# Kernel optimization log

Measured on AMD Instinct MI355X. Metric: run time of the kernel, lower is better.

## Reference

```python
import jax, jax.numpy as jnp
import numpy as np

B, S, D = 4, 4096, 1024

def setup_inputs() -> dict:
    key = jax.random.key(0)
    ks = jax.random.split(key, 11)
    scale = 1.0 / np.sqrt(D)
    def lin(k):
        return jax.random.normal(k, (D, D), dtype=jnp.float32) * scale
    return {
        "x": jax.random.normal(ks[0], (B, S, D), dtype=jnp.float32),
        "Wq": lin(ks[1]), "bq": jax.random.normal(ks[2], (D,), dtype=jnp.float32) * 0.02,
        "Wk": lin(ks[3]), "bk": jax.random.normal(ks[4], (D,), dtype=jnp.float32) * 0.02,
        "Wv": lin(ks[5]), "bv": jax.random.normal(ks[6], (D,), dtype=jnp.float32) * 0.02,
        "W1": lin(ks[7]), "b1": jax.random.normal(ks[8], (D,), dtype=jnp.float32) * 0.02,
        "W2": lin(ks[9]), "b2": jax.random.normal(ks[10], (D,), dtype=jnp.float32) * 0.02,
    }

def reference(x, Wq, bq, Wk, bk, Wv, bv, W1, b1, W2, b2):
    d = x.shape[-1]
    # Single-head self-attention with residual (faithful to source)
    q = x @ Wq + bq  # [B,S,D]
    k = x @ Wk + bk
    v = x @ Wv + bv
    scores = jnp.einsum('bsd,btd->bst', q, k) / jnp.sqrt(jnp.float32(d))  # [B,S,S]
    attn = jax.nn.softmax(scores, axis=-1)
    x = x + jnp.einsum('bst,btd->bsd', attn, v)
    # FeedForward: fc2(relu(fc1(x))), then doubled (x = x + x in source)
    h = jax.nn.relu(x @ W1 + b1)
    y = h @ W2 + b2
    return y + y
```

## Files before the change

kernel.cpp:

```cpp
#include <hip/hip_runtime.h>
#include <stdint.h>

typedef unsigned short u16;
typedef __bf16 bf16x8 __attribute__((ext_vector_type(8)));
typedef float f32x4 __attribute__((ext_vector_type(4)));
typedef unsigned short u16x8 __attribute__((ext_vector_type(8)));
typedef unsigned short u16x4 __attribute__((ext_vector_type(4)));

__device__ __forceinline__ float b2f(u16 b) {
    return __uint_as_float(((unsigned)b) << 16);
}
__device__ __forceinline__ u16 f2b(float f) {
    unsigned u = __float_as_uint(f);
    unsigned r = (u + 0x7fffu + ((u >> 16) & 1u)) >> 16;
    return (u16)r;
}

#define GLDS16(g, l) __builtin_amdgcn_global_load_lds(                        \
    (const __attribute__((address_space(1))) void*)(g),                       \
    (__attribute__((address_space(3))) void*)(l), 16, 0, 0)

template<int HAS_BIAS, int RELU, int HAS_RES, int OUT_MODE>
__device__ __forceinline__ void gemm11_body(
    const u16* __restrict__ A, const u16* __restrict__ Bt,
    const float* __restrict__ bias, const float* __restrict__ res,
    void* __restrict__ Cout, int N, int K,
    long sA, long sB, long sC, long sR, float scale)
{
    __shared__ u16 smem[65536];

    const long nwg = (long)gridDim.x * gridDim.y * gridDim.z;
    long gid = ((long)blockIdx.z * gridDim.y + blockIdx.y) * gridDim.x + blockIdx.x;
    long logical = (nwg % 8 == 0) ? (gid & 7) * (nwg >> 3) + (gid >> 3) : gid;
    const int bx = (int)(logical % gridDim.x);
    long tmp = logical / gridDim.x;
    const int by = (int)(tmp % gridDim.y);
    const int bz = (int)(tmp / gridDim.y);

    A  += (long)bz * sA;
    Bt += (long)bz * sB;

    const int tid  = threadIdx.x;
    const int lane = tid & 63, wid = tid >> 6;
    const int wm   = wid >> 2, wn = wid & 3;
    const int lr   = lane & 15, lk = lane >> 4;
    const long m0  = (long)by * 256;
    const long n0  = (long)bx * 256;
    const int  NT  = K >> 6;

    const int sch = ((tid & 3) ^ ((tid >> 3) & 3)) * 8;
    const u16* gA0 = A  + (m0 + (tid >> 2)) * (long)K + sch;
    const u16* gB0 = Bt + (n0 + (tid >> 2)) * (long)K + sch;
    const u16* gA1 = gA0 + 128L * K;
    const u16* gB1 = gB0 + 128L * K;
    const int wdst = (tid & ~63) * 8;

#define STA(bufn, kk, kof) do {                                               \
    GLDS16(gA0 + (kof) + (kk) * 32, &smem[(bufn)*16384 + (kk)*8192 + wdst]);  \
    GLDS16(gA1 + (kof) + (kk) * 32, &smem[(bufn)*16384 + (kk)*8192 + wdst + 4096]); } while (0)
#define STB(bufn, kk, kof) do {                                               \
    GLDS16(gB0 + (kof) + (kk) * 32, &smem[32768 + (bufn)*16384 + (kk)*8192 + wdst]); \
    GLDS16(gB1 + (kof) + (kk) * 32, &smem[32768 + (bufn)*16384 + (kk)*8192 + wdst + 4096]); } while (0)

    const int lkA   = lk ^ ((lr >> 1) & 3);
    const int raOff = (wm * 128 + lr) * 32 + lkA * 8;
    const int rbOff = (wn * 64  + lr) * 32 + lkA * 8;

#define DSA(dst, BUF, kk, ih) do { _Pragma("unroll")                          \
    for (int i = 0; i < 4; ++i)                                               \
        dst[i] = *(const bf16x8*)&smem[(BUF)*16384 + (kk)*8192 + raOff + ((ih)*4 + i)*512]; } while (0)
#define DSB(dst, BUF, kk) do { _Pragma("unroll")                              \
    for (int j = 0; j < 4; ++j)                                               \
        dst[j] = *(const bf16x8*)&smem[32768 + (BUF)*16384 + (kk)*8192 + rbOff + j*512]; } while (0)

#define LGK(n) do { asm volatile("s_waitcnt lgkmcnt(" #n ")" ::: "memory");   \
                    __builtin_amdgcn_sched_barrier(0); } while (0)
#define CKPT(n) do { asm volatile("s_waitcnt vmcnt(" #n ")" ::: "memory");    \
    __builtin_amdgcn_s_barrier(); __builtin_amdgcn_sched_barrier(0); } while (0)

#define MFM(IH, A_, B_) do { __builtin_amdgcn_s_setprio(1); _Pragma("unroll") \
    for (int i = 0; i < 4; ++i) _Pragma("unroll")                             \
        for (int j = 0; j < 4; ++j)                                           \
            acc[(IH)*4 + i][j] = __builtin_amdgcn_mfma_f32_16x16x32_bf16(     \
                A_[i], B_[j], acc[(IH)*4 + i][j], 0, 0, 0);                   \
    __builtin_amdgcn_s_setprio(0); } while (0)

#define TILE_MAIN(BUF, kof) do {                                              \
    DSA(aY, BUF, 0, 1);                 STA((BUF)^1, 0, kof);                 \
    LGK(4);  MFM(0, aX, bX);                                                  \
    CKPT(2);                                                                  \
    DSA(aX, BUF, 1, 0);  DSB(bY, BUF, 1);  STB((BUF)^1, 0, kof);              \
    LGK(8);  MFM(1, aY, bX);                                                  \
    DSA(aY, BUF, 1, 1);                 STA((BUF)^1, 1, kof);                 \
    LGK(4);  MFM(0, aX, bY);                                                  \
    CKPT(2);                                                                  \
    DSA(aX, (BUF)^1, 0, 0);  DSB(bX, (BUF)^1, 0);  STB((BUF)^1, 1, kof);      \
    LGK(8);  MFM(1, aY, bY);                                                  \
} while (0)

#define TILE_LAST(BUF) do {                                                   \
    DSA(aY, BUF, 0, 1);                                                       \
    LGK(4);  MFM(0, aX, bX);                                                  \
    CKPT(0);                                                                  \
    DSA(aX, BUF, 1, 0);  DSB(bY, BUF, 1);                                     \
    LGK(8);  MFM(1, aY, bX);                                                  \
    DSA(aY, BUF, 1, 1);                                                       \
    LGK(4);  MFM(0, aX, bY);                                                  \
    LGK(0);  MFM(1, aY, bY);                                                  \
} while (0)

    f32x4 acc[8][4];
    #pragma unroll
    for (int i = 0; i < 8; ++i)
        #pragma unroll
        for (int j = 0; j < 4; ++j)
            #pragma unroll
            for (int r = 0; r < 4; ++r) acc[i][j][r] = 0.0f;

    bf16x8 aX[4], aY[4], bX[4], bY[4];

    STA(0, 0, 0); STB(0, 0, 0); STA(0, 1, 0); STB(0, 1, 0);
    CKPT(4);
    DSA(aX, 0, 0, 0); DSB(bX, 0, 0);

    #pragma unroll 1
    for (int t = 0; t + 2 < NT; t += 2) {
        TILE_MAIN(0, (long)(t + 1) * 64);
        TILE_MAIN(1, (long)(t + 2) * 64);
    }
    TILE_MAIN(0, (long)(NT - 1) * 64);
    TILE_LAST(1);

    const long crow0 = m0 + wm * 128;
    const long ccol0 = n0 + wn * 64;
    u16*   Cb = (u16*)Cout   + (long)bz * sC;
    float* Cf = (float*)Cout + (long)bz * sC;
    const float* resz = res + (long)bz * sR;
    #pragma unroll
    for (int i = 0; i < 8; ++i) {
        #pragma unroll
        for (int j = 0; j < 4; ++j) {
            const long col = ccol0 + j * 16 + lr;
            float bv_ = 0.0f;
            if (HAS_BIAS) bv_ = bias[col];
            if (OUT_MODE == 2) {
                const long row0 = crow0 + i * 16 + lk * 4;
                u16x4 pk;
                #pragma unroll
                for (int r = 0; r < 4; ++r) {
                    float v = acc[i][j][r] + bv_;
                    v *= scale;
                    pk[r] = f2b(v);
                }
                const long b_ = row0 >> 12, s_ = row0 & 4095;
                *(u16x4*)((u16*)Cout + (b_ << 22) + (col << 12) + s_) = pk;
            } else {
                #pragma unroll
                for (int r = 0; r < 4; ++r) {
                    const long row = crow0 + i * 16 + lk * 4 + r;
                    float v = acc[i][j][r];
                    if (HAS_BIAS) v += bv_;
                    v *= scale;
                    if (RELU) v = fmaxf(v, 0.0f);
                    if (HAS_RES) v += resz[row * (long)N + col];
                    if (OUT_MODE == 1) Cf[row * (long)N + col] = v;
                    else               Cb[row * (long)N + col] = f2b(v);
                }
            }
        }
    }
#undef STA
#undef STB
#undef DSA
#undef DSB
#undef LGK
#undef CKPT
#undef MFM
#undef TILE_MAIN
#undef TILE_LAST
}

__global__ __launch_bounds__(512, 2) void g11_proj(
    const u16* A, const u16* Bt, const float* bias, u16* C, int N, int K)
{ gemm11_body<1,0,0,0>(A, Bt, bias, nullptr, C, N, K, 0,0,0,0, 1.0f); }

__global__ __launch_bounds__(512, 2) void g11_vproj(
    const u16* A, const u16* Bt, const float* bias, u16* C, int N, int K)
{ gemm11_body<1,0,0,2>(A, Bt, bias, nullptr, C, N, K, 0,0,0,0, 1.0f); }

__global__ __launch_bounds__(512, 2) void g11_qkt(
    const u16* A, const u16* Bt, u16* C, int N, int K,
    long sA, long sB, long sC, float scale)
{ gemm11_body<0,0,0,0>(A, Bt, nullptr, nullptr, C, N, K, sA, sB, sC, 0, scale); }

__global__ __launch_bounds__(512, 2) void g11_pv(
    const u16* A, const u16* Bt, const float* res, u16* C, int N, int K,
    long sA, long sB, long sC, long sR)
{ gemm11_body<0,0,1,0>(A, Bt, nullptr, res, C, N, K, sA, sB, sC, sR, 1.0f); }

__global__ __launch_bounds__(512, 2) void g11_ffn1(
    const u16* A, const u16* Bt, const float* bias, u16* C, int N, int K)
{ gemm11_body<1,1,0,0>(A, Bt, bias, nullptr, C, N, K, 0,0,0,0, 1.0f); }

__global__ __launch_bounds__(512, 2) void g11_ffn2(
    const u16* A, const u16* Bt, const float* bias, float* C, int N, int K, float scale)
{ gemm11_body<1,0,0,1>(A, Bt, bias, nullptr, C, N, K, 0,0,0,0, scale); }

__global__ __launch_bounds__(256) void cvt_f32_bf16(
    const float* __restrict__ in, u16* __restrict__ out, long n)
{
    long i = ((long)blockIdx.x * 256 + threadIdx.x) * 4;
    if (i >= n) return;
    float4 f = *(const float4*)(in + i);
    u16x4 o;
    o[0] = f2b(f.x); o[1] = f2b(f.y); o[2] = f2b(f.z); o[3] = f2b(f.w);
    *(u16x4*)(out + i) = o;
}

__global__ __launch_bounds__(256) void transpose_to_bf16(
    const float* __restrict__ in, u16* __restrict__ out, int R, int C)
{
    __shared__ float tile[32][33];
    const int bx = blockIdx.x * 32;
    const int by = blockIdx.y * 32;
    const int tx = threadIdx.x, ty = threadIdx.y;
    #pragma unroll
    for (int i = 0; i < 32; i += 8)
        tile[ty + i][tx] = in[(long)(by + ty + i) * C + bx + tx];
    __syncthreads();
    #pragma unroll
    for (int i = 0; i < 32; i += 8)
        out[(long)(bx + ty + i) * R + by + tx] = f2b(tile[tx][ty + i]);
}

__global__ __launch_bounds__(256) void softmax_rows(u16* __restrict__ P, int n)
{
    const int t = threadIdx.x;
    const int lane = t & 63, w = t >> 6;
    u16* row = P + (long)blockIdx.x * n;
    u16x8 a = *(const u16x8*)(row + t * 16);
    u16x8 b = *(const u16x8*)(row + t * 16 + 8);
    float v[16];
    #pragma unroll
    for (int i = 0; i < 8; ++i) { v[i] = b2f(a[i]); v[8 + i] = b2f(b[i]); }

    float mx = v[0];
    #pragma unroll
    for (int i = 1; i < 16; ++i) mx = fmaxf(mx, v[i]);
    #pragma unroll
    for (int o = 32; o > 0; o >>= 1) mx = fmaxf(mx, __shfl_xor(mx, o));
    __shared__ float red[8];
    if (lane == 0) red[w] = mx;
    __syncthreads();
    mx = fmaxf(fmaxf(red[0], red[1]), fmaxf(red[2], red[3]));

    float s = 0.0f;
    #pragma unroll
    for (int i = 0; i < 16; ++i) { v[i] = __expf(v[i] - mx); s += v[i]; }
    #pragma unroll
    for (int o = 32; o > 0; o >>= 1) s += __shfl_xor(s, o);
    if (lane == 0) red[4 + w] = s;
    __syncthreads();
    s = red[4] + red[5] + red[6] + red[7];
    const float inv = 1.0f / s;

    #pragma unroll
    for (int i = 0; i < 8; ++i) { a[i] = f2b(v[i] * inv); b[i] = f2b(v[8 + i] * inv); }
    *(u16x8*)(row + t * 16)     = a;
    *(u16x8*)(row + t * 16 + 8) = b;
}

extern "C" void kernel_launch(void* const* d_in, const int* in_sizes, int n_in,
                              void* d_out, int out_size, void* d_ws, size_t ws_size,
                              hipStream_t stream)
{
    (void)in_sizes; (void)n_in; (void)out_size;
    const float* x  = (const float*)d_in[0];
    const float* Wq = (const float*)d_in[1];
    const float* bq = (const float*)d_in[2];
    const float* Wk = (const float*)d_in[3];
    const float* bk = (const float*)d_in[4];
    const float* Wv = (const float*)d_in[5];
    const float* bv = (const float*)d_in[6];
    const float* W1 = (const float*)d_in[7];
    const float* b1 = (const float*)d_in[8];
    const float* W2 = (const float*)d_in[9];
    const float* b2 = (const float*)d_in[10];
    float* out = (float*)d_out;

    const int  B = 4, S = 4096, D = 1024;
    const long SD  = (long)S * D;
    const long BSD = (long)B * SD;
    const long SS  = (long)S * S;

    int BC = 4;
    while (BC > 1 && (size_t)((long)BC * SS + 5L * D * D + 3L * BSD) * 2 > ws_size)
        BC >>= 1;

    u16* Pb = (u16*)d_ws;
    u16* xb = Pb;
    u16* Wt = Pb + (long)BC * SS;
    u16* Qb = Wt + 5L * D * D;
    u16* Kb = Qb + BSD;
    u16* Vt = Kb + BSD;

    cvt_f32_bf16<<<dim3((unsigned)(BSD / 4 / 256)), 256, 0, stream>>>(x, xb, BSD);

    dim3 tb(32, 8);
    transpose_to_bf16<<<dim3(D / 32, D / 32), tb, 0, stream>>>(Wq, Wt + 0L * D * D, D, D);
    transpose_to_bf16<<<dim3(D / 32, D / 32), tb, 0, stream>>>(Wk, Wt + 1L * D * D, D, D);
    transpose_to_bf16<<<dim3(D / 32, D / 32), tb, 0, stream>>>(Wv, Wt + 2L * D * D, D, D);
    transpose_to_bf16<<<dim3(D / 32, D / 32), tb, 0, stream>>>(W1, Wt + 3L * D * D, D, D);
    transpose_to_bf16<<<dim3(D / 32, D / 32), tb, 0, stream>>>(W2, Wt + 4L * D * D, D, D);

    const dim3 gproj(D / 256, (B * S) / 256);
    g11_proj <<<gproj, 512, 0, stream>>>(xb, Wt + 0L*D*D, bq, Qb, D, D);
    g11_proj <<<gproj, 512, 0, stream>>>(xb, Wt + 1L*D*D, bk, Kb, D, D);
    g11_vproj<<<gproj, 512, 0, stream>>>(xb, Wt + 2L*D*D, bv, Vt, D, D);

    for (int c = 0; c < B; c += BC) {
        g11_qkt<<<dim3(S/256, S/256, BC), 512, 0, stream>>>(
            Qb + (long)c * SD, Kb + (long)c * SD, Pb, S, D, SD, SD, SS, 0.03125f);
        softmax_rows<<<BC * S, 256, 0, stream>>>(Pb, S);
        g11_pv<<<dim3(D/256, S/256, BC), 512, 0, stream>>>(
            Pb, Vt + (long)c * SD, x + (long)c * SD, Kb + (long)c * SD,
            D, S, SS, SD, SD, SD);
    }

    g11_ffn1<<<gproj, 512, 0, stream>>>(Kb, Wt + 3L*D*D, b1, Qb, D, D);
    g11_ffn2<<<gproj, 512, 0, stream>>>(Qb, Wt + 4L*D*D, b2, out, D, D, 2.0f);
}
```

Baseline: 530.7 us.

## Switch GEMM inner loop from 16x16x32 to 32x32x16 bf16 MFMA tiles

Replaces the 16x16x32 MFMA microkernel with 32x32x16 MFMA instructions across all GEMM stages. The LDS read pattern, swizzle offsets, accumulator layout and epilogue row/column mapping are rewritten to match the larger instruction's operand and output layout. Each wave now issues fewer MFMAs and fewer B-fragment LDS reads per K step, which raises data reuse per LDS read. The risk is a different register footprint and LDS bank behavior under the existing swizzle.

```diff
diff --git a/kernel.cpp b/kernel.cpp
--- a/kernel.cpp
+++ b/kernel.cpp
@@ -4,6 +4,7 @@
 typedef unsigned short u16;
 typedef __bf16 bf16x8 __attribute__((ext_vector_type(8)));
 typedef float f32x4 __attribute__((ext_vector_type(4)));
+typedef float f32x16 __attribute__((ext_vector_type(16)));
 typedef unsigned short u16x8 __attribute__((ext_vector_type(8)));
 typedef unsigned short u16x4 __attribute__((ext_vector_type(4)));
 
@@ -21,7 +22,7 @@
     (__attribute__((address_space(3))) void*)(l), 16, 0, 0)
 
 template<int HAS_BIAS, int RELU, int HAS_RES, int OUT_MODE>
-__device__ __forceinline__ void gemm11_body(
+__device__ __forceinline__ void gemm12_body(
     const u16* __restrict__ A, const u16* __restrict__ Bt,
     const float* __restrict__ bias, const float* __restrict__ res,
     void* __restrict__ Cout, int N, int K,
@@ -43,7 +44,7 @@
     const int tid  = threadIdx.x;
     const int lane = tid & 63, wid = tid >> 6;
     const int wm   = wid >> 2, wn = wid & 3;
-    const int lr   = lane & 15, lk = lane >> 4;
+    const int lr32 = lane & 31, lk2 = lane >> 5;
     const long m0  = (long)by * 256;
     const long n0  = (long)bx * 256;
     const int  NT  = K >> 6;
@@ -62,66 +63,70 @@
     GLDS16(gB0 + (kof) + (kk) * 32, &smem[32768 + (bufn)*16384 + (kk)*8192 + wdst]); \
     GLDS16(gB1 + (kof) + (kk) * 32, &smem[32768 + (bufn)*16384 + (kk)*8192 + wdst + 4096]); } while (0)
 
-    const int lkA   = lk ^ ((lr >> 1) & 3);
-    const int raOff = (wm * 128 + lr) * 32 + lkA * 8;
-    const int rbOff = (wn * 64  + lr) * 32 + lkA * 8;
-
-#define DSA(dst, BUF, kk, ih) do { _Pragma("unroll")                          \
-    for (int i = 0; i < 4; ++i)                                               \
-        dst[i] = *(const bf16x8*)&smem[(BUF)*16384 + (kk)*8192 + raOff + ((ih)*4 + i)*512]; } while (0)
-#define DSB(dst, BUF, kk) do { _Pragma("unroll")                              \
-    for (int j = 0; j < 4; ++j)                                               \
-        dst[j] = *(const bf16x8*)&smem[32768 + (BUF)*16384 + (kk)*8192 + rbOff + j*512]; } while (0)
+    const int m_   = (lr32 >> 1) & 3;
+    const int cOff = ((lk2 ^ m_) << 3);
+    int aBase[4], bBase[2];
+    #pragma unroll
+    for (int mb = 0; mb < 4; ++mb) aBase[mb] = (wm * 128 + mb * 32 + lr32) * 32;
+    #pragma unroll
+    for (int nb = 0; nb < 2; ++nb) bBase[nb] = (wn * 64 + nb * 32 + lr32) * 32;
+
+#define DSAS(dst, BUF, S) do { _Pragma("unroll")                              \
+    for (int mb = 0; mb < 4; ++mb)                                            \
+        dst[mb] = *(const bf16x8*)&smem[(BUF)*16384 + ((S)>>1)*8192 +         \
+                                        aBase[mb] + (cOff ^ (((S)&1)<<4))]; } while (0)
+#define DSBS(dst, BUF, S) do { _Pragma("unroll")                              \
+    for (int nb = 0; nb < 2; ++nb)                                            \
+        dst[nb] = *(const bf16x8*)&smem[32768 + (BUF)*16384 + ((S)>>1)*8192 + \
+                                        bBase[nb] + (cOff ^ (((S)&1)<<4))]; } while (0)
 
 #define LGK(n) do { asm volatile("s_waitcnt lgkmcnt(" #n ")" ::: "memory");   \
                     __builtin_amdgcn_sched_barrier(0); } while (0)
 #define CKPT(n) do { asm volatile("s_waitcnt vmcnt(" #n ")" ::: "memory");    \
     __builtin_amdgcn_s_barrier(); __builtin_amdgcn_sched_barrier(0); } while (0)
 
-#define MFM(IH, A_, B_) do { __builtin_amdgcn_s_setprio(1); _Pragma("unroll") \
-    for (int i = 0; i < 4; ++i) _Pragma("unroll")                             \
-        for (int j = 0; j < 4; ++j)                                           \
-            acc[(IH)*4 + i][j] = __builtin_amdgcn_mfma_f32_16x16x32_bf16(     \
-                A_[i], B_[j], acc[(IH)*4 + i][j], 0, 0, 0);                   \
+#define MFM8(A_, B_) do { __builtin_amdgcn_s_setprio(1); _Pragma("unroll")    \
+    for (int mb = 0; mb < 4; ++mb) _Pragma("unroll")                          \
+        for (int nb = 0; nb < 2; ++nb)                                        \
+            acc[mb * 2 + nb] = __builtin_amdgcn_mfma_f32_32x32x16_bf16(       \
+                A_[mb], B_[nb], acc[mb * 2 + nb], 0, 0, 0);                   \
     __builtin_amdgcn_s_setprio(0); } while (0)
 
 #define TILE_MAIN(BUF, kof) do {                                              \
-    DSA(aY, BUF, 0, 1);                 STA((BUF)^1, 0, kof);                 \
-    LGK(4);  MFM(0, aX, bX);                                                  \
+    DSAS(aY, BUF, 1);  DSBS(bY, BUF, 1);  STA((BUF)^1, 0, kof);               \
+    LGK(6);  MFM8(aX, bX);                                                    \
     CKPT(2);                                                                  \
-    DSA(aX, BUF, 1, 0);  DSB(bY, BUF, 1);  STB((BUF)^1, 0, kof);              \
-    LGK(8);  MFM(1, aY, bX);                                                  \
-    DSA(aY, BUF, 1, 1);                 STA((BUF)^1, 1, kof);                 \
-    LGK(4);  MFM(0, aX, bY);                                                  \
+    DSAS(aX, BUF, 2);  DSBS(bX, BUF, 2);  STB((BUF)^1, 0, kof);               \
+    LGK(6);  MFM8(aY, bY);                                                    \
+    DSAS(aY, BUF, 3);  DSBS(bY, BUF, 3);  STA((BUF)^1, 1, kof);               \
+    LGK(6);  MFM8(aX, bX);                                                    \
     CKPT(2);                                                                  \
-    DSA(aX, (BUF)^1, 0, 0);  DSB(bX, (BUF)^1, 0);  STB((BUF)^1, 1, kof);      \
-    LGK(8);  MFM(1, aY, bY);                                                  \
+    DSAS(aX, (BUF)^1, 0);  DSBS(bX, (BUF)^1, 0);  STB((BUF)^1, 1, kof);       \
+    LGK(6);  MFM8(aY, bY);                                                    \
 } while (0)
 
 #define TILE_LAST(BUF) do {                                                   \
-    DSA(aY, BUF, 0, 1);                                                       \
-    LGK(4);  MFM(0, aX, bX);                                                  \
+    DSAS(aY, BUF, 1);  DSBS(bY, BUF, 1);                                      \
+    LGK(6);  MFM8(aX, bX);                                                    \
     CKPT(0);                                                                  \
-    DSA(aX, BUF, 1, 0);  DSB(bY, BUF, 1);                                     \
-    LGK(8);  MFM(1, aY, bX);                                                  \
-    DSA(aY, BUF, 1, 1);                                                       \
-    LGK(4);  MFM(0, aX, bY);                                                  \
-    LGK(0);  MFM(1, aY, bY);                                                  \
+    DSAS(aX, BUF, 2);  DSBS(bX, BUF, 2);                                      \
+    LGK(6);  MFM8(aY, bY);                                                    \
+    DSAS(aY, BUF, 3);  DSBS(bY, BUF, 3);                                      \
+    LGK(6);  MFM8(aX, bX);                                                    \
+    LGK(0);  MFM8(aY, bY);                                                    \
 } while (0)
 
-    f32x4 acc[8][4];
-    #pragma unroll
-    for (int i = 0; i < 8; ++i)
+    f32x16 acc[8];
+    #pragma unroll
+    for (int b = 0; b < 8; ++b)
         #pragma unroll
-        for (int j = 0; j < 4; ++j)
-            #pragma unroll
-            for (int r = 0; r < 4; ++r) acc[i][j][r] = 0.0f;
-
-    bf16x8 aX[4], aY[4], bX[4], bY[4];
+        for (int r = 0; r < 16; ++r) acc[b][r] = 0.0f;
+
+    bf16x8 aX[4], aY[4], bX[2], bY[2];
 
     STA(0, 0, 0); STB(0, 0, 0); STA(0, 1, 0); STB(0, 1, 0);
     CKPT(4);
-    DSA(aX, 0, 0, 0); DSB(bX, 0, 0);
+    DSAS(aX, 0, 0); DSBS(bX, 0, 0);
 
     #pragma unroll 1
     for (int t = 0; t + 2 < NT; t += 2) {
@@ -137,74 +142,80 @@
     float* Cf = (float*)Cout + (long)bz * sC;
     const float* resz = res + (long)bz * sR;
     #pragma unroll
-    for (int i = 0; i < 8; ++i) {
+    for (int mb = 0; mb < 4; ++mb) {
         #pragma unroll
-        for (int j = 0; j < 4; ++j) {
-            const long col = ccol0 + j * 16 + lr;
+        for (int nb = 0; nb < 2; ++nb) {
+            const long col = ccol0 + nb * 32 + lr32;
             float bv_ = 0.0f;
             if (HAS_BIAS) bv_ = bias[col];
             if (OUT_MODE == 2) {
-                const long row0 = crow0 + i * 16 + lk * 4;
-                u16x4 pk;
                 #pragma unroll
-                for (int r = 0; r < 4; ++r) {
-                    float v = acc[i][j][r] + bv_;
-                    v *= scale;
-                    pk[r] = f2b(v);
+                for (int rq = 0; rq < 4; ++rq) {
+                    const long row0 = crow0 + mb * 32 + rq * 8 + lk2 * 4;
+                    u16x4 pk;
+                    #pragma unroll
+                    for (int r = 0; r < 4; ++r) {
+                        float v = acc[mb * 2 + nb][rq * 4 + r] + bv_;
+                        v *= scale;
+                        pk[r] = f2b(v);
+                    }
+                    const long b_ = row0 >> 12, s_ = row0 & 4095;
+                    *(u16x4*)((u16*)Cout + (b_ << 22) + (col << 12) + s_) = pk;
                 }
-                const long b_ = row0 >> 12, s_ = row0 & 4095;
-                *(u16x4*)((u16*)Cout + (b_ << 22) + (col << 12) + s_) = pk;
             } else {
                 #pragma unroll
-                for (int r = 0; r < 4; ++r) {
-                    const long row = crow0 + i * 16 + lk * 4 + r;
-                    float v = acc[i][j][r];
-                    if (HAS_BIAS) v += bv_;
-                    v *= scale;
-                    if (RELU) v = fmaxf(v, 0.0f);
-                    if (HAS_RES) v += resz[row * (long)N + col];
-                    if (OUT_MODE == 1) Cf[row * (long)N + col] = v;
-                    else               Cb[row * (long)N + col] = f2b(v);
+                for (int rq = 0; rq < 4; ++rq) {
+                    #pragma unroll
+                    for (int r = 0; r < 4; ++r) {
+                        const long row = crow0 + mb * 32 + rq * 8 + lk2 * 4 + r;
+                        float v = acc[mb * 2 + nb][rq * 4 + r];
+                        if (HAS_BIAS) v += bv_;
+                        v *= scale;
+                        if (RELU) v = fmaxf(v, 0.0f);
+                        if (HAS_RES) v += resz[row * (long)N + col];
+                        if (OUT_MODE == 1) Cf[row * (long)N + col] = v;
+                        else               Cb[row * (long)N + col] = f2b(v);
+                    }
                 }
             }
         }
     }
 #undef STA
 #undef STB
-#undef DSA
-#undef DSB
+#undef DSAS
+#undef DSBS
 #undef LGK
 #undef CKPT
-#undef MFM
+#undef MFM8
 #undef TILE_MAIN
 #undef TILE_LAST
 }
 
-__global__ __launch_bounds__(512, 2) void g11_proj(
+__global__ __launch_bounds__(512, 2) void g12_proj(
     const u16* A, const u16* Bt, const float* bias, u16* C, int N, int K)
-{ gemm11_body<1,0,0,0>(A, Bt, bias, nullptr, C, N, K, 0,0,0,0, 1.0f); }
-
-__global__ __launch_bounds__(512, 2) void g11_vproj(
+{ gemm12_body<1,0,0,0>(A, Bt, bias, nullptr, C, N, K, 0,0,0,0, 1.0f); }
+
+__global__ __launch_bounds__(512, 2) void g12_vproj(
     const u16* A, const u16* Bt, const float* bias, u16* C, int N, int K)
-{ gemm11_body<1,0,0,2>(A, Bt, bias, nullptr, C, N, K, 0,0,0,0, 1.0f); }
-
-__global__ __launch_bounds__(512, 2) void g11_qkt(
+{ gemm12_body<1,0,0,2>(A, Bt, bias, nullptr, C, N, K, 0,0,0,0, 1.0f); }
+
+__global__ __launch_bounds__(512, 2) void g12_qkt(
     const u16* A, const u16* Bt, u16* C, int N, int K,
     long sA, long sB, long sC, float scale)
-{ gemm11_body<0,0,0,0>(A, Bt, nullptr, nullptr, C, N, K, sA, sB, sC, 0, scale); }
-
-__global__ __launch_bounds__(512, 2) void g11_pv(
+{ gemm12_body<0,0,0,0>(A, Bt, nullptr, nullptr, C, N, K, sA, sB, sC, 0, scale); }
+
+__global__ __launch_bounds__(512, 2) void g12_pv(
     const u16* A, const u16* Bt, const float* res, u16* C, int N, int K,
     long sA, long sB, long sC, long sR)
-{ gemm11_body<0,0,1,0>(A, Bt, nullptr, res, C, N, K, sA, sB, sC, sR, 1.0f); }
-
-__global__ __launch_bounds__(512, 2) void g11_ffn1(
+{ gemm12_body<0,0,1,0>(A, Bt, nullptr, res, C, N, K, sA, sB, sC, sR, 1.0f); }
+
+__global__ __launch_bounds__(512, 2) void g12_ffn1(
     const u16* A, const u16* Bt, const float* bias, u16* C, int N, int K)
-{ gemm11_body<1,1,0,0>(A, Bt, bias, nullptr, C, N, K, 0,0,0,0, 1.0f); }
-
-__global__ __launch_bounds__(512, 2) void g11_ffn2(
+{ gemm12_body<1,1,0,0>(A, Bt, bias, nullptr, C, N, K, 0,0,0,0, 1.0f); }
+
+__global__ __launch_bounds__(512, 2) void g12_ffn2(
     const u16* A, const u16* Bt, const float* bias, float* C, int N, int K, float scale)
-{ gemm11_body<1,0,0,1>(A, Bt, bias, nullptr, C, N, K, 0,0,0,0, scale); }
+{ gemm12_body<1,0,0,1>(A, Bt, bias, nullptr, C, N, K, 0,0,0,0, scale); }
 
 __global__ __launch_bounds__(256) void cvt_f32_bf16(
     const float* __restrict__ in, u16* __restrict__ out, long n)
@@ -314,19 +325,19 @@
     transpose_to_bf16<<<dim3(D / 32, D / 32), tb, 0, stream>>>(W2, Wt + 4L * D * D, D, D);
 
     const dim3 gproj(D / 256, (B * S) / 256);
-    g11_proj <<<gproj, 512, 0, stream>>>(xb, Wt + 0L*D*D, bq, Qb, D, D);
-    g11_proj <<<gproj, 512, 0, stream>>>(xb, Wt + 1L*D*D, bk, Kb, D, D);
-    g11_vproj<<<gproj, 512, 0, stream>>>(xb, Wt + 2L*D*D, bv, Vt, D, D);
+    g12_proj <<<gproj, 512, 0, stream>>>(xb, Wt + 0L*D*D, bq, Qb, D, D);
+    g12_proj <<<gproj, 512, 0, stream>>>(xb, Wt + 1L*D*D, bk, Kb, D, D);
+    g12_vproj<<<gproj, 512, 0, stream>>>(xb, Wt + 2L*D*D, bv, Vt, D, D);
 
     for (int c = 0; c < B; c += BC) {
-        g11_qkt<<<dim3(S/256, S/256, BC), 512, 0, stream>>>(
+        g12_qkt<<<dim3(S/256, S/256, BC), 512, 0, stream>>>(
             Qb + (long)c * SD, Kb + (long)c * SD, Pb, S, D, SD, SD, SS, 0.03125f);
         softmax_rows<<<BC * S, 256, 0, stream>>>(Pb, S);
-        g11_pv<<<dim3(D/256, S/256, BC), 512, 0, stream>>>(
+        g12_pv<<<dim3(D/256, S/256, BC), 512, 0, stream>>>(
             Pb, Vt + (long)c * SD, x + (long)c * SD, Kb + (long)c * SD,
             D, S, SS, SD, SD, SD);
     }
 
-    g11_ffn1<<<gproj, 512, 0, stream>>>(Kb, Wt + 3L*D*D, b1, Qb, D, D);
-    g11_ffn2<<<gproj, 512, 0, stream>>>(Qb, Wt + 4L*D*D, b2, out, D, D, 2.0f);
-}
+    g12_ffn1<<<gproj, 512, 0, stream>>>(Kb, Wt + 3L*D*D, b1, Qb, D, D);
+    g12_ffn2<<<gproj, 512, 0, stream>>>(Qb, Wt + 4L*D*D, b2, out, D, D, 2.0f);
+}
```

After: 536.3 us. Within noise of the previous version (+1.1%).

## Fuse Q/K/V projections into one GEMM and batch weight transposes

Applied to the files above, without the earlier changes.

The three separate Q, K and V projection launches become one GEMM over the concatenated transposed weights, with N=3072. The epilogue routes each 1024-column slice to Q, K (row-major) or transposed V and picks the matching bias. The five weight transposes are merged into one launch using blockIdx.z, and the s_setprio hints around the MFMA blocks are removed. This cuts launch count and gives one larger grid for better CU fill, at the cost of a branchier epilogue. It relies on Qb, Kb and Vt lying contiguously in the workspace, 16M elements apart.

```diff
diff --git a/kernel.cpp b/kernel.cpp
--- a/kernel.cpp
+++ b/kernel.cpp
@@ -21,9 +21,10 @@
     (__attribute__((address_space(3))) void*)(l), 16, 0, 0)
 
 template<int HAS_BIAS, int RELU, int HAS_RES, int OUT_MODE>
-__device__ __forceinline__ void gemm11_body(
+__device__ __forceinline__ void gemm16_body(
     const u16* __restrict__ A, const u16* __restrict__ Bt,
-    const float* __restrict__ bias, const float* __restrict__ res,
+    const float* __restrict__ bias, const float* __restrict__ bias2,
+    const float* __restrict__ bias3, const float* __restrict__ res,
     void* __restrict__ Cout, int N, int K,
     long sA, long sB, long sC, long sR, float scale)
 {
@@ -78,12 +79,12 @@
 #define CKPT(n) do { asm volatile("s_waitcnt vmcnt(" #n ")" ::: "memory");    \
     __builtin_amdgcn_s_barrier(); __builtin_amdgcn_sched_barrier(0); } while (0)
 
-#define MFM(IH, A_, B_) do { __builtin_amdgcn_s_setprio(1); _Pragma("unroll") \
+#define MFM(IH, A_, B_) do { _Pragma("unroll")                                \
     for (int i = 0; i < 4; ++i) _Pragma("unroll")                             \
         for (int j = 0; j < 4; ++j)                                           \
             acc[(IH)*4 + i][j] = __builtin_amdgcn_mfma_f32_16x16x32_bf16(     \
                 A_[i], B_[j], acc[(IH)*4 + i][j], 0, 0, 0);                   \
-    __builtin_amdgcn_s_setprio(0); } while (0)
+} while (0)
 
 #define TILE_MAIN(BUF, kof) do {                                              \
     DSA(aY, BUF, 0, 1);                 STA((BUF)^1, 0, kof);                 \
@@ -136,11 +137,36 @@
     u16*   Cb = (u16*)Cout   + (long)bz * sC;
     float* Cf = (float*)Cout + (long)bz * sC;
     const float* resz = res + (long)bz * sR;
+    const int sel = (OUT_MODE == 3) ? (int)(n0 >> 10) : 0;
+    const float* bp3 = (OUT_MODE == 3)
+        ? (sel == 0 ? bias : (sel == 1 ? bias2 : bias3)) : nullptr;
+    u16* qk3 = (OUT_MODE == 3) ? ((u16*)Cout + ((long)sel << 24)) : nullptr;
+    u16* vt3 = (OUT_MODE == 3) ? ((u16*)Cout + (2L << 24)) : nullptr;
+
     #pragma unroll
     for (int i = 0; i < 8; ++i) {
         #pragma unroll
         for (int j = 0; j < 4; ++j) {
             const long col = ccol0 + j * 16 + lr;
+            if (OUT_MODE == 3) {
+                const long c10 = col & 1023;
+                const float bv_ = bp3[c10];
+                if (sel < 2) {
+                    #pragma unroll
+                    for (int r = 0; r < 4; ++r) {
+                        const long row = crow0 + i * 16 + lk * 4 + r;
+                        qk3[row * 1024 + c10] = f2b(acc[i][j][r] + bv_);
+                    }
+                } else {
+                    const long row0 = crow0 + i * 16 + lk * 4;
+                    u16x4 pk;
+                    #pragma unroll
+                    for (int r = 0; r < 4; ++r) pk[r] = f2b(acc[i][j][r] + bv_);
+                    const long b_ = row0 >> 12, s_ = row0 & 4095;
+                    *(u16x4*)(vt3 + (b_ << 22) + (c10 << 12) + s_) = pk;
+                }
+                continue;
+            }
             float bv_ = 0.0f;
             if (HAS_BIAS) bv_ = bias[col];
             if (OUT_MODE == 2) {
@@ -180,31 +206,28 @@
 #undef TILE_LAST
 }
 
-__global__ __launch_bounds__(512, 2) void g11_proj(
-    const u16* A, const u16* Bt, const float* bias, u16* C, int N, int K)
-{ gemm11_body<1,0,0,0>(A, Bt, bias, nullptr, C, N, K, 0,0,0,0, 1.0f); }
-
-__global__ __launch_bounds__(512, 2) void g11_vproj(
-    const u16* A, const u16* Bt, const float* bias, u16* C, int N, int K)
-{ gemm11_body<1,0,0,2>(A, Bt, bias, nullptr, C, N, K, 0,0,0,0, 1.0f); }
-
-__global__ __launch_bounds__(512, 2) void g11_qkt(
+__global__ __launch_bounds__(512, 2) void g16_qkv(
+    const u16* A, const u16* Bt, const float* bq, const float* bk,
+    const float* bv, u16* Qb, int K)
+{ gemm16_body<1,0,0,3>(A, Bt, bq, bk, bv, nullptr, Qb, 1024, K, 0,0,0,0, 1.0f); }
+
+__global__ __launch_bounds__(512, 2) void g16_qkt(
     const u16* A, const u16* Bt, u16* C, int N, int K,
     long sA, long sB, long sC, float scale)
-{ gemm11_body<0,0,0,0>(A, Bt, nullptr, nullptr, C, N, K, sA, sB, sC, 0, scale); }
-
-__global__ __launch_bounds__(512, 2) void g11_pv(
+{ gemm16_body<0,0,0,0>(A, Bt, nullptr, nullptr, nullptr, nullptr, C, N, K, sA, sB, sC, 0, scale); }
+
+__global__ __launch_bounds__(512, 2) void g16_pv(
     const u16* A, const u16* Bt, const float* res, u16* C, int N, int K,
     long sA, long sB, long sC, long sR)
-{ gemm11_body<0,0,1,0>(A, Bt, nullptr, res, C, N, K, sA, sB, sC, sR, 1.0f); }
-
-__global__ __launch_bounds__(512, 2) void g11_ffn1(
+{ gemm16_body<0,0,1,0>(A, Bt, nullptr, nullptr, nullptr, res, C, N, K, sA, sB, sC, sR, 1.0f); }
+
+__global__ __launch_bounds__(512, 2) void g16_ffn1(
     const u16* A, const u16* Bt, const float* bias, u16* C, int N, int K)
-{ gemm11_body<1,1,0,0>(A, Bt, bias, nullptr, C, N, K, 0,0,0,0, 1.0f); }
-
-__global__ __launch_bounds__(512, 2) void g11_ffn2(
+{ gemm16_body<1,1,0,0>(A, Bt, bias, nullptr, nullptr, nullptr, C, N, K, 0,0,0,0, 1.0f); }
+
+__global__ __launch_bounds__(512, 2) void g16_ffn2(
     const u16* A, const u16* Bt, const float* bias, float* C, int N, int K, float scale)
-{ gemm11_body<1,0,0,1>(A, Bt, bias, nullptr, C, N, K, 0,0,0,0, scale); }
+{ gemm16_body<1,0,0,1>(A, Bt, bias, nullptr, nullptr, nullptr, C, N, K, 0,0,0,0, scale); }
 
 __global__ __launch_bounds__(256) void cvt_f32_bf16(
     const float* __restrict__ in, u16* __restrict__ out, long n)
@@ -217,20 +240,26 @@
     *(u16x4*)(out + i) = o;
 }
 
-__global__ __launch_bounds__(256) void transpose_to_bf16(
-    const float* __restrict__ in, u16* __restrict__ out, int R, int C)
-{
+__global__ __launch_bounds__(256) void transpose5_to_bf16(
+    const float* __restrict__ Wq, const float* __restrict__ Wk,
+    const float* __restrict__ Wv, const float* __restrict__ W1,
+    const float* __restrict__ W2, u16* __restrict__ out, int Dm)
+{
+    const int z = blockIdx.z;
+    const float* in = (z == 0) ? Wq : (z == 1) ? Wk : (z == 2) ? Wv
+                    : (z == 3) ? W1 : W2;
+    u16* o = out + (long)z * Dm * Dm;
     __shared__ float tile[32][33];
     const int bx = blockIdx.x * 32;
     const int by = blockIdx.y * 32;
     const int tx = threadIdx.x, ty = threadIdx.y;
     #pragma unroll
     for (int i = 0; i < 32; i += 8)
-        tile[ty + i][tx] = in[(long)(by + ty + i) * C + bx + tx];
+        tile[ty + i][tx] = in[(long)(by + ty + i) * Dm + bx + tx];
     __syncthreads();
     #pragma unroll
     for (int i = 0; i < 32; i += 8)
-        out[(long)(bx + ty + i) * R + by + tx] = f2b(tile[tx][ty + i]);
+        o[(long)(bx + ty + i) * Dm + by + tx] = f2b(tile[tx][ty + i]);
 }
 
 __global__ __launch_bounds__(256) void softmax_rows(u16* __restrict__ P, int n)
@@ -306,27 +335,22 @@
 
     cvt_f32_bf16<<<dim3((unsigned)(BSD / 4 / 256)), 256, 0, stream>>>(x, xb, BSD);
 
-    dim3 tb(32, 8);
-    transpose_to_bf16<<<dim3(D / 32, D / 32), tb, 0, stream>>>(Wq, Wt + 0L * D * D, D, D);
-    transpose_to_bf16<<<dim3(D / 32, D / 32), tb, 0, stream>>>(Wk, Wt + 1L * D * D, D, D);
-    transpose_to_bf16<<<dim3(D / 32, D / 32), tb, 0, stream>>>(Wv, Wt + 2L * D * D, D, D);
-    transpose_to_bf16<<<dim3(D / 32, D / 32), tb, 0, stream>>>(W1, Wt + 3L * D * D, D, D);
-    transpose_to_bf16<<<dim3(D / 32, D / 32), tb, 0, stream>>>(W2, Wt + 4L * D * D, D, D);
-
-    const dim3 gproj(D / 256, (B * S) / 256);
-    g11_proj <<<gproj, 512, 0, stream>>>(xb, Wt + 0L*D*D, bq, Qb, D, D);
-    g11_proj <<<gproj, 512, 0, stream>>>(xb, Wt + 1L*D*D, bk, Kb, D, D);
-    g11_vproj<<<gproj, 512, 0, stream>>>(xb, Wt + 2L*D*D, bv, Vt, D, D);
+    transpose5_to_bf16<<<dim3(D / 32, D / 32, 5), dim3(32, 8), 0, stream>>>(
+        Wq, Wk, Wv, W1, W2, Wt, D);
+
+    g16_qkv<<<dim3(3 * D / 256, (B * S) / 256), 512, 0, stream>>>(
+        xb, Wt, bq, bk, bv, Qb, D);
 
     for (int c = 0; c < B; c += BC) {
-        g11_qkt<<<dim3(S/256, S/256, BC), 512, 0, stream>>>(
+        g16_qkt<<<dim3(S/256, S/256, BC), 512, 0, stream>>>(
             Qb + (long)c * SD, Kb + (long)c * SD, Pb, S, D, SD, SD, SS, 0.03125f);
         softmax_rows<<<BC * S, 256, 0, stream>>>(Pb, S);
-        g11_pv<<<dim3(D/256, S/256, BC), 512, 0, stream>>>(
+        g16_pv<<<dim3(D/256, S/256, BC), 512, 0, stream>>>(
             Pb, Vt + (long)c * SD, x + (long)c * SD, Kb + (long)c * SD,
             D, S, SS, SD, SD, SD);
     }
 
-    g11_ffn1<<<gproj, 512, 0, stream>>>(Kb, Wt + 3L*D*D, b1, Qb, D, D);
-    g11_ffn2<<<gproj, 512, 0, stream>>>(Qb, Wt + 4L*D*D, b2, out, D, D, 2.0f);
-}
+    const dim3 gproj(D / 256, (B * S) / 256);
+    g16_ffn1<<<gproj, 512, 0, stream>>>(Kb, Wt + 3L*D*D, b1, Qb, D, D);
+    g16_ffn2<<<gproj, 512, 0, stream>>>(Qb, Wt + 4L*D*D, b2, out, D, D, 2.0f);
+}
```

Result: slower. 556.9 us (+4.9%).
